# Kernel tuning notes

Measured on AMD Instinct MI355X. Metric: run time of the kernel, lower is better.

## Reference

```python
import jax, jax.numpy as jnp
import numpy as np

ROUTINGS = 3
EPS = 1e-7  # K.epsilon()


def squash(s, axis=-1):
    # v = (||s||^2 / (1 + ||s||^2)) * s / ||s||
    s_sq = jnp.sum(jnp.square(s), axis=axis, keepdims=True)
    scale = s_sq / (1.0 + s_sq) / jnp.sqrt(s_sq + EPS)
    return scale * s


def setup_inputs() -> dict:
    key = jax.random.key(0)
    k1, k2 = jax.random.split(key)
    B, num_in_caps, in_caps_dim = 32, 2048, 16
    num_caps, caps_dim = 64, 32
    input_tensor = jax.random.normal(k1, (B, num_in_caps, in_caps_dim), dtype=jnp.float32)
    # he_normal init: std = sqrt(2 / fan_in), fan_in = in_caps_dim (last axis contracted)
    fan_in = num_in_caps * caps_dim * in_caps_dim  # keras computes fan_in from receptive field; use simple he scale
    W = jax.random.normal(k2, (num_caps, num_in_caps, caps_dim, in_caps_dim), dtype=jnp.float32) * np.float32(np.sqrt(2.0 / in_caps_dim))
    return {"input_tensor": input_tensor, "W": W}


def reference(input_tensor, W):
    B = input_tensor.shape[0]
    num_caps, num_in_caps = W.shape[0], W.shape[1]
    # inputs_hat[b,j,i,c] = sum_d W[j,i,c,d] * x[b,i,d]  (fused einsum replacing map_fn+batch_dot)
    inputs_hat = jnp.einsum('bid,jicd->bjic', input_tensor, W)
    b = jnp.zeros((B, num_caps, num_in_caps), dtype=inputs_hat.dtype)
    # NOTE: source never updates b inside the loop, so every iteration is identical.
    activations = None
    for _ in range(ROUTINGS):
        c = jax.nn.softmax(b, axis=1)  # over num_caps axis, as tf.nn.softmax(b, dim=1)
        s = jnp.einsum('bji,bjic->bjc', c, inputs_hat)  # batch_dot(c, inputs_hat, [2,2])
        activations = squash(s)
    return activations
```

## Files before the change

kernel.cpp:

```cpp
#include <hip/hip_runtime.h>

typedef __attribute__((ext_vector_type(8)))  short bf16x8;
typedef __attribute__((ext_vector_type(16))) float f32x16;
typedef __attribute__((ext_vector_type(4)))  int   i32x4;

__device__ __forceinline__ unsigned cvt2(float lo, float hi) {
    unsigned r;
    asm volatile("v_cvt_pk_bf16_f32 %0, %1, %2" : "=v"(r) : "v"(lo), "v"(hi));
    return r;
}
__device__ __forceinline__ bf16x8 pack8(float4 a, float4 b) {
    union { i32x4 i; bf16x8 h; } c;
    c.i.x = cvt2(a.x, a.y);
    c.i.y = cvt2(a.z, a.w);
    c.i.z = cvt2(b.x, b.y);
    c.i.w = cvt2(b.z, b.w);
    return c.h;
}

__global__ void caps_xconv(const float* __restrict__ x, uint4* __restrict__ xf) {
    int g = blockIdx.x * 256 + threadIdx.x;
    int i = g >> 6, l = g & 63;
    int b = l & 31, h = l >> 5;
    const float4* p = (const float4*)(x + (b * 2048 + i) * 16 + h * 8);
    float4 a = p[0], q = p[1];
    uint4 o;
    o.x = cvt2(a.x, a.y); o.y = cvt2(a.z, a.w);
    o.z = cvt2(q.x, q.y); o.w = cvt2(q.z, q.w);
    xf[g] = o;
}

__global__ void caps_init(float* __restrict__ ws) {
    ws[blockIdx.x * 256 + threadIdx.x] = 0.0f;
}

template<int MODE, int GATHER, int ICHUNK>
__global__ __launch_bounds__(256, 4)
void caps_mfma(const float* __restrict__ x, const float* __restrict__ W,
               float* __restrict__ ws, const char* __restrict__ xf)
{
    constexpr int NIC = 2048 / ICHUNK;
    constexpr int NT  = ICHUNK / 4;

    const int tid  = threadIdx.x;
    const int w    = tid >> 6;
    const int lane = tid & 63;
    const int m    = lane & 31;
    const int h    = lane >> 5;

    const int j     = blockIdx.x / NIC;
    const int ic    = blockIdx.x % NIC;
    const int ibase = ic * ICHUNK;

    const char* Wb = (const char*)W + (((size_t)(j * 2048 + ibase + w)) << 11)
                   + (m << 6) + (h << 5);
    const char* Xb = (const char*)x + ((size_t)m << 17) + ((ibase + w) << 6) + (h << 5);
    const char* Xf = xf + ((ibase + w) << 10) + (lane << 4);

    f32x16 acc = {};

    float4 wv[4][2];
    bf16x8 xa[4];
    float4 xg[4][2];

#pragma unroll
    for (int s = 0; s < 4; ++s) {
        wv[s][0] = *(const float4*)(Wb + s * 8192);
        wv[s][1] = *(const float4*)(Wb + s * 8192 + 16);
        if (GATHER) {
            xg[s][0] = *(const float4*)(Xb + s * 256);
            xg[s][1] = *(const float4*)(Xb + s * 256 + 16);
        } else {
            xa[s] = *(const bf16x8*)(Xf + s * 4096);
        }
    }

#pragma unroll 1
    for (int t = 0; t < NT - 4; t += 4) {
#pragma unroll
        for (int s = 0; s < 4; ++s) {
            bf16x8 afrag = GATHER ? pack8(xg[s][0], xg[s][1]) : xa[s];
            bf16x8 bfrag = pack8(wv[s][0], wv[s][1]);
            wv[s][0] = *(const float4*)(Wb + (s + 4) * 8192);
            wv[s][1] = *(const float4*)(Wb + (s + 4) * 8192 + 16);
            if (GATHER) {
                xg[s][0] = *(const float4*)(Xb + (s + 4) * 256);
                xg[s][1] = *(const float4*)(Xb + (s + 4) * 256 + 16);
            } else {
                xa[s] = *(const bf16x8*)(Xf + (s + 4) * 4096);
            }
            acc = __builtin_amdgcn_mfma_f32_32x32x16_bf16(afrag, bfrag, acc, 0, 0, 0);
        }
        Wb += 4 * 8192; Xb += 4 * 256; Xf += 4 * 4096;
    }
#pragma unroll
    for (int s = 0; s < 4; ++s) {
        bf16x8 afrag = GATHER ? pack8(xg[s][0], xg[s][1]) : xa[s];
        acc = __builtin_amdgcn_mfma_f32_32x32x16_bf16(
                  afrag, pack8(wv[s][0], wv[s][1]), acc, 0, 0, 0);
    }

    __shared__ float red[4096];
#pragma unroll
    for (int r = 0; r < 16; ++r)
        red[w * 1024 + r * 64 + lane] = acc[r];
    __syncthreads();

#pragma unroll
    for (int e = 0; e < 4; ++e) {
        int idx = e * 256 + tid;
        int b = idx >> 5, c = idx & 31;
        int l = (((b >> 2) & 1) << 5) + c;
        int r = (b & 3) | (((b >> 3) & 3) << 2);
        float s = red[r * 64 + l] + red[1024 + r * 64 + l]
                + red[2048 + r * 64 + l] + red[3072 + r * 64 + l];
        if (MODE == 0)
            ws[(ic * 32 + b) * 2048 + j * 32 + c] = s;
        else
            atomicAdd(&ws[b * 2048 + j * 32 + c], s);
    }
}

template<int NIC>
__global__ void caps_finalize(const float* __restrict__ ws, float* __restrict__ out) {
    int o = blockIdx.x * 256 + threadIdx.x;
    int b = o >> 11;
    int rest = o & 2047;
    float v = 0.0f;
#pragma unroll
    for (int k = 0; k < NIC; ++k) v += ws[(k * 32 + b) * 2048 + rest];
    v *= (1.0f / 64.0f);
    float sq = v * v;
    sq += __shfl_xor(sq, 1, 64);
    sq += __shfl_xor(sq, 2, 64);
    sq += __shfl_xor(sq, 4, 64);
    sq += __shfl_xor(sq, 8, 64);
    sq += __shfl_xor(sq, 16, 64);
    float scale = sq / (1.0f + sq) / sqrtf(sq + 1e-7f);
    out[o] = scale * v;
}

__global__ void caps_finalize_a(const float* __restrict__ ws, float* __restrict__ out) {
    int o = blockIdx.x * 256 + threadIdx.x;
    float v = ws[o] * (1.0f / 64.0f);
    float sq = v * v;
    sq += __shfl_xor(sq, 1, 64);
    sq += __shfl_xor(sq, 2, 64);
    sq += __shfl_xor(sq, 4, 64);
    sq += __shfl_xor(sq, 8, 64);
    sq += __shfl_xor(sq, 16, 64);
    float scale = sq / (1.0f + sq) / sqrtf(sq + 1e-7f);
    out[o] = scale * v;
}

extern "C" void kernel_launch(void* const* d_in, const int* in_sizes, int n_in,
                              void* d_out, int out_size, void* d_ws, size_t ws_size,
                              hipStream_t stream) {
    (void)in_sizes; (void)n_in; (void)out_size;
    const float* x = (const float*)d_in[0];
    const float* W = (const float*)d_in[1];
    float* out = (float*)d_out;
    float* ws  = (float*)d_ws;

    const size_t slab_f = (size_t)32 * 32 * 2048;
    const size_t need   = slab_f * 4 + (size_t)2048 * 1024;

    if (ws_size >= need) {
        char* xf = (char*)(ws + slab_f);
        hipLaunchKernelGGL(caps_xconv,            dim3(512),  dim3(256), 0, stream, x, (uint4*)xf);
        hipLaunchKernelGGL((caps_mfma<0, 0, 64>), dim3(2048), dim3(256), 0, stream, x, W, ws, xf);
        hipLaunchKernelGGL((caps_finalize<32>),   dim3(256),  dim3(256), 0, stream, ws, out);
    } else if (ws_size >= (size_t)16 * 65536 * sizeof(float)) {
        hipLaunchKernelGGL((caps_mfma<0, 1, 128>), dim3(1024), dim3(256), 0, stream, x, W, ws, (const char*)0);
        hipLaunchKernelGGL((caps_finalize<16>),    dim3(256),  dim3(256), 0, stream, ws, out);
    } else {
        float* acc_buf = (ws_size >= (size_t)65536 * sizeof(float)) ? ws : out;
        hipLaunchKernelGGL(caps_init,              dim3(256),  dim3(256), 0, stream, acc_buf);
        hipLaunchKernelGGL((caps_mfma<1, 1, 128>), dim3(1024), dim3(256), 0, stream, x, W, acc_buf, (const char*)0);
        hipLaunchKernelGGL(caps_finalize_a,        dim3(256),  dim3(256), 0, stream, acc_buf, out);
    }
}
```

Baseline: 52.87 us.

## Shrink W prefetch depth to two stages and use 128-wide input chunks

Cuts the register prefetch pipeline in the MFMA kernel from four in-flight stages to two. The default path now uses 128-input-capsule chunks, which halves the grid to 1024 blocks, halves the partial-sum slab and the finalize reduction (16 slabs), and lowers the workspace requirement. The aim is less register pressure and less partial-sum traffic. The cost is fewer blocks for hiding memory latency and less load-ahead per wave on a kernel bound by streaming W.

Result: no change. 53.41 us (+1.0%).

```diff
diff --git a/kernel.cpp b/kernel.cpp
--- a/kernel.cpp
+++ b/kernel.cpp
@@ -59,46 +59,52 @@
 
     f32x16 acc = {};
 
-    float4 wv[4][2];
-    bf16x8 xa[4];
-    float4 xg[4][2];
-
-#pragma unroll
-    for (int s = 0; s < 4; ++s) {
-        wv[s][0] = *(const float4*)(Wb + s * 8192);
-        wv[s][1] = *(const float4*)(Wb + s * 8192 + 16);
-        if (GATHER) {
-            xg[s][0] = *(const float4*)(Xb + s * 256);
-            xg[s][1] = *(const float4*)(Xb + s * 256 + 16);
-        } else {
-            xa[s] = *(const bf16x8*)(Xf + s * 4096);
-        }
+    float4 wA0 = *(const float4*)(Wb);
+    float4 wA1 = *(const float4*)(Wb + 16);
+    float4 wB0 = *(const float4*)(Wb + 8192);
+    float4 wB1 = *(const float4*)(Wb + 8192 + 16);
+    bf16x8 xA, xB;
+    float4 gA0, gA1, gB0, gB1;
+    if (GATHER) {
+        gA0 = *(const float4*)(Xb);       gA1 = *(const float4*)(Xb + 16);
+        gB0 = *(const float4*)(Xb + 256); gB1 = *(const float4*)(Xb + 256 + 16);
+    } else {
+        xA = *(const bf16x8*)(Xf);
+        xB = *(const bf16x8*)(Xf + 4096);
     }
 
 #pragma unroll 1
-    for (int t = 0; t < NT - 4; t += 4) {
-#pragma unroll
-        for (int s = 0; s < 4; ++s) {
-            bf16x8 afrag = GATHER ? pack8(xg[s][0], xg[s][1]) : xa[s];
-            bf16x8 bfrag = pack8(wv[s][0], wv[s][1]);
-            wv[s][0] = *(const float4*)(Wb + (s + 4) * 8192);
-            wv[s][1] = *(const float4*)(Wb + (s + 4) * 8192 + 16);
-            if (GATHER) {
-                xg[s][0] = *(const float4*)(Xb + (s + 4) * 256);
-                xg[s][1] = *(const float4*)(Xb + (s + 4) * 256 + 16);
-            } else {
-                xa[s] = *(const bf16x8*)(Xf + (s + 4) * 4096);
-            }
-            acc = __builtin_amdgcn_mfma_f32_32x32x16_bf16(afrag, bfrag, acc, 0, 0, 0);
+    for (int t = 0; t < NT - 2; t += 2) {
+        bf16x8 a  = GATHER ? pack8(gA0, gA1) : xA;
+        bf16x8 fa = pack8(wA0, wA1);
+        wA0 = *(const float4*)(Wb + 16384);
+        wA1 = *(const float4*)(Wb + 16384 + 16);
+        if (GATHER) {
+            gA0 = *(const float4*)(Xb + 512);
+            gA1 = *(const float4*)(Xb + 512 + 16);
+        } else {
+            xA = *(const bf16x8*)(Xf + 8192);
         }
-        Wb += 4 * 8192; Xb += 4 * 256; Xf += 4 * 4096;
+        acc = __builtin_amdgcn_mfma_f32_32x32x16_bf16(a, fa, acc, 0, 0, 0);
+
+        bf16x8 b  = GATHER ? pack8(gB0, gB1) : xB;
+        bf16x8 fb = pack8(wB0, wB1);
+        wB0 = *(const float4*)(Wb + 24576);
+        wB1 = *(const float4*)(Wb + 24576 + 16);
+        if (GATHER) {
+            gB0 = *(const float4*)(Xb + 768);
+            gB1 = *(const float4*)(Xb + 768 + 16);
+        } else {
+            xB = *(const bf16x8*)(Xf + 12288);
+        }
+        acc = __builtin_amdgcn_mfma_f32_32x32x16_bf16(b, fb, acc, 0, 0, 0);
+
+        Wb += 16384; Xb += 512; Xf += 8192;
     }
-#pragma unroll
-    for (int s = 0; s < 4; ++s) {
-        bf16x8 afrag = GATHER ? pack8(xg[s][0], xg[s][1]) : xa[s];
-        acc = __builtin_amdgcn_mfma_f32_32x32x16_bf16(
-                  afrag, pack8(wv[s][0], wv[s][1]), acc, 0, 0, 0);
-    }
+    acc = __builtin_amdgcn_mfma_f32_32x32x16_bf16(
+              GATHER ? pack8(gA0, gA1) : xA, pack8(wA0, wA1), acc, 0, 0, 0);
+    acc = __builtin_amdgcn_mfma_f32_32x32x16_bf16(
+              GATHER ? pack8(gB0, gB1) : xB, pack8(wB0, wB1), acc, 0, 0, 0);
 
     __shared__ float red[4096];
 #pragma unroll
@@ -162,15 +168,15 @@
     float* out = (float*)d_out;
     float* ws  = (float*)d_ws;
 
-    const size_t slab_f = (size_t)32 * 32 * 2048;
+    const size_t slab_f = (size_t)16 * 32 * 2048;
     const size_t need   = slab_f * 4 + (size_t)2048 * 1024;
 
     if (ws_size >= need) {
         char* xf = (char*)(ws + slab_f);
-        hipLaunchKernelGGL(caps_xconv,            dim3(512),  dim3(256), 0, stream, x, (uint4*)xf);
-        hipLaunchKernelGGL((caps_mfma<0, 0, 64>), dim3(2048), dim3(256), 0, stream, x, W, ws, xf);
-        hipLaunchKernelGGL((caps_finalize<32>),   dim3(256),  dim3(256), 0, stream, ws, out);
-    } else if (ws_size >= (size_t)16 * 65536 * sizeof(float)) {
+        hipLaunchKernelGGL(caps_xconv,             dim3(512),  dim3(256), 0, stream, x, (uint4*)xf);
+        hipLaunchKernelGGL((caps_mfma<0, 0, 128>), dim3(1024), dim3(256), 0, stream, x, W, ws, xf);
+        hipLaunchKernelGGL((caps_finalize<16>),    dim3(256),  dim3(256), 0, stream, ws, out);
+    } else if (ws_size >= slab_f * 4) {
         hipLaunchKernelGGL((caps_mfma<0, 1, 128>), dim3(1024), dim3(256), 0, stream, x, W, ws, (const char*)0);
         hipLaunchKernelGGL((caps_finalize<16>),    dim3(256),  dim3(256), 0, stream, ws, out);
     } else {
```
